# Performance work log

Hardware: AMD Instinct MI355X
Metric: run time of the kernel (lower is better)

## Reference

```python
import jax, jax.numpy as jnp
import numpy as np

B, S, D = 8, 2048, 512  # batch, seq_len, dim_val == dim_attn

def setup_inputs() -> dict:
    key = jax.random.key(0)
    kx, kq, kk, kv = jax.random.split(key, 4)
    scale = 1.0 / np.sqrt(D)
    return {
        "x": jax.random.normal(kx, (B, S, D), dtype=jnp.float32),
        "Wq": jax.random.normal(kq, (D, D), dtype=jnp.float32) * scale,  # dim_input -> dim_attn
        "Wk": jax.random.normal(kk, (D, D), dtype=jnp.float32) * scale,
        "Wv": jax.random.normal(kv, (D, D), dtype=jnp.float32) * scale,  # dim_input -> dim_val
    }

def reference(x, Wq, Wk, Wv):
    # bias-free linear projections (nn.Linear stores W as [out,in]; here W is [in,out])
    Q = jnp.einsum("bsd,de->bse", x, Wq)
    K = jnp.einsum("bsd,de->bse", x, Wk)
    V = jnp.einsum("bsd,de->bse", x, Wv)
    # manual scaled dot-product attention: softmax(QK^T / sqrt(d_attn)) V
    scores = jnp.einsum("bqe,bke->bqk", Q, K) / jnp.sqrt(jnp.asarray(Q.shape[-1], Q.dtype))
    a = jax.nn.softmax(scores, axis=-1)
    return jnp.einsum("bqk,bkd->bqd", a, V)
```

## Files before the change

### kernel.cpp

```cpp
#include <hip/hip_runtime.h>


typedef __attribute__((ext_vector_type(8))) short bf16x8;
typedef __attribute__((ext_vector_type(4))) short short4v;
typedef __attribute__((ext_vector_type(4))) float f32x4;
typedef __attribute__((ext_vector_type(16))) float f32x16;

__device__ __forceinline__ short f2bf(float f) {
  union { float f; unsigned u; } v; v.f = f;
  unsigned r = v.u + 0x7fffu + ((v.u >> 16) & 1u);
  return (short)(r >> 16);
}

__device__ __forceinline__ float exp2_raw(float x) {
  float r;
  asm("v_exp_f32 %0, %1" : "=v"(r) : "v"(x));
  return r;
}

__global__ __launch_bounds__(256) void prep_kernel(const float* __restrict__ x,
                                                   const float* __restrict__ Wq,
                                                   const float* __restrict__ Wk,
                                                   const float* __restrict__ Wv,
                                                   short* __restrict__ WT,
                                                   short* __restrict__ xb) {
  if (blockIdx.x < 384) {
    int g = blockIdx.x * 256 + threadIdx.x;
    int w = g >> 15;
    int rem = g & 32767;
    int n = rem & 511;
    int k0 = (rem >> 9) << 3;
    const float* W = (w == 0) ? Wq : ((w == 1) ? Wk : Wv);
    bf16x8 o;
#pragma unroll
    for (int j = 0; j < 8; ++j) o[j] = f2bf(W[(k0 + j) * 512 + n]);
    *(bf16x8*)(WT + w * 262144 + n * 512 + k0) = o;
  } else {
    size_t g = (size_t)(blockIdx.x - 384) * 256 + threadIdx.x;
    size_t off = g * 8;
    f32x4 lo = *(const f32x4*)(x + off);
    f32x4 hi = *(const f32x4*)(x + off + 4);
    bf16x8 o;
    o[0] = f2bf(lo[0]); o[1] = f2bf(lo[1]); o[2] = f2bf(lo[2]); o[3] = f2bf(lo[3]);
    o[4] = f2bf(hi[0]); o[5] = f2bf(hi[1]); o[6] = f2bf(hi[2]); o[7] = f2bf(hi[3]);
    *(bf16x8*)(xb + off) = o;
  }
}

__global__ __launch_bounds__(256, 2) void proj_kernel(const short* __restrict__ xb,
                                                      const short* __restrict__ WT,
                                                      short* __restrict__ QP,
                                                      short* __restrict__ KP,
                                                      short* __restrict__ VP) {
  __shared__ __align__(16) short Tb[8704];

  const int tid = threadIdx.x, wv = tid >> 6, ln = tid & 63;
  const int lane_m = ln & 15, lane_q = ln >> 4;
  const int m0 = blockIdx.x * 128, n0 = blockIdx.y * 64;
  const int wm = wv & 1, wn = wv >> 1;

  const short* ap[4];
#pragma unroll
  for (int mi = 0; mi < 4; ++mi)
    ap[mi] = xb + (size_t)(m0 + (wm * 4 + mi) * 16 + lane_m) * 512 + lane_q * 8;
  const short* bp[3][2];
#pragma unroll
  for (int z = 0; z < 3; ++z)
#pragma unroll
    for (int nj = 0; nj < 2; ++nj)
      bp[z][nj] = WT + z * 262144 + (size_t)(n0 + (wn * 2 + nj) * 16 + lane_m) * 512 + lane_q * 8;

  f32x4 zero4 = {0.f, 0.f, 0.f, 0.f};
  f32x4 acc[3][4][2];
#pragma unroll
  for (int z = 0; z < 3; ++z)
#pragma unroll
    for (int i = 0; i < 4; ++i)
#pragma unroll
      for (int j = 0; j < 2; ++j) acc[z][i][j] = zero4;

#pragma unroll
  for (int kk = 0; kk < 16; ++kk) {
    const int ko = kk * 32;
    bf16x8 a[4];
#pragma unroll
    for (int mi = 0; mi < 4; ++mi) a[mi] = *(const bf16x8*)(ap[mi] + ko);
    bf16x8 b[3][2];
#pragma unroll
    for (int z = 0; z < 3; ++z)
#pragma unroll
      for (int nj = 0; nj < 2; ++nj) b[z][nj] = *(const bf16x8*)(bp[z][nj] + ko);
#pragma unroll
    for (int z = 0; z < 3; ++z)
#pragma unroll
      for (int mi = 0; mi < 4; ++mi) {
        acc[z][mi][0] = __builtin_amdgcn_mfma_f32_16x16x32_bf16(a[mi], b[z][0], acc[z][mi][0], 0, 0, 0);
        acc[z][mi][1] = __builtin_amdgcn_mfma_f32_16x16x32_bf16(a[mi], b[z][1], acc[z][mi][1], 0, 0, 0);
      }
  }

  const int bb = m0 >> 11;

#pragma unroll
  for (int z = 0; z < 2; ++z) {
    __syncthreads();
#pragma unroll
    for (int mi = 0; mi < 4; ++mi)
#pragma unroll
      for (int nj = 0; nj < 2; ++nj)
#pragma unroll
        for (int rr = 0; rr < 4; ++rr)
          Tb[(wm * 64 + mi * 16 + lane_q * 4 + rr) * 68 + wn * 32 + nj * 16 + lane_m] =
              f2bf(acc[z][mi][nj][rr]);
    __syncthreads();
    short* Odst = (z == 0) ? QP : KP;
    const int g0 = (m0 & 2047) >> 5, kst0 = n0 >> 4;
#pragma unroll
    for (int p = 0; p < 4; ++p) {
      const int c2 = p * 256 + tid;
      const int frag = c2 >> 6, ln2 = c2 & 63;
      const int gl = frag >> 2, kl = frag & 3;
      const short* src = Tb + (gl * 32 + (ln2 & 31)) * 68 + kl * 16 + ((ln2 >> 5) << 3);
      size_t dst = (size_t)bb * 1048576 + (size_t)((g0 + gl) * 32 + kst0 + kl) * 512 + ln2 * 8;
      *(bf16x8*)(Odst + dst) = *(const bf16x8*)src;
    }
  }
  {
    __syncthreads();
#pragma unroll
    for (int mi = 0; mi < 4; ++mi)
#pragma unroll
      for (int nj = 0; nj < 2; ++nj)
#pragma unroll
        for (int rr = 0; rr < 4; ++rr)
          Tb[(wn * 32 + nj * 16 + lane_m) * 132 + wm * 64 + mi * 16 + lane_q * 4 + rr] =
              f2bf(acc[2][mi][nj][rr]);
    __syncthreads();
    const int ng0 = n0 >> 5, kv0 = (m0 & 2047) >> 4;
#pragma unroll
    for (int p = 0; p < 4; ++p) {
      const int c2 = p * 256 + tid;
      const int frag = c2 >> 6, ln2 = c2 & 63;
      const int ngl = frag >> 3, kvl = frag & 7;
      const short* src = Tb + (ngl * 32 + (ln2 & 31)) * 132 + kvl * 16 + ((ln2 >> 5) << 3);
      size_t dst = (size_t)bb * 1048576 + (size_t)((ng0 + ngl) * 128 + kv0 + kvl) * 512 + ln2 * 8;
      *(bf16x8*)(VP + dst) = *(const bf16x8*)src;
    }
  }
}


#define ISSUE8(R, a0_, a1_, B)                                               \
  asm volatile("global_load_dwordx4 %0, %8, %10\n\t"                         \
               "global_load_dwordx4 %1, %8, %10 offset:1024\n\t"             \
               "global_load_dwordx4 %2, %8, %10 offset:2048\n\t"             \
               "global_load_dwordx4 %3, %8, %10 offset:3072\n\t"             \
               "global_load_dwordx4 %4, %9, %10\n\t"                         \
               "global_load_dwordx4 %5, %9, %10 offset:1024\n\t"             \
               "global_load_dwordx4 %6, %9, %10 offset:2048\n\t"             \
               "global_load_dwordx4 %7, %9, %10 offset:3072\n\t"             \
               : "=&v"(R[0]), "=&v"(R[1]), "=&v"(R[2]), "=&v"(R[3]),         \
                 "=&v"(R[4]), "=&v"(R[5]), "=&v"(R[6]), "=&v"(R[7])          \
               : "v"(a0_), "v"(a1_), "s"(B))

#define WAIT8(R, N)                                                          \
  asm volatile("s_waitcnt vmcnt(" #N ")"                                     \
               : "+v"(R[0]), "+v"(R[1]), "+v"(R[2]), "+v"(R[3]),             \
                 "+v"(R[4]), "+v"(R[5]), "+v"(R[6]), "+v"(R[7]))

#define MFMA32(A, B, C) __builtin_amdgcn_mfma_f32_32x32x16_bf16(A, B, C, 0, 0, 0)

#define ISSUE_KQ(X, kt_, qq)                                                 \
  { const unsigned a0 = kb0 + (unsigned)(((kt_) & 7) * 262144) + (qq) * 8192u; \
    ISSUE8(X, a0, a0 + 4096u, Kp); }

#define ISSUE_VQ(X, kt_, bb_)                                                \
  { const unsigned a0 = vb0 + (unsigned)((kt_) * 16384) + (bb_) * 4096u;     \
    ISSUE8(X, a0, a0 + 131072u, VTp); }

#define S_PHASE(X, ph)                                                       \
  WAIT8(X, 8);                                                               \
  __builtin_amdgcn_s_setprio(1);                                             \
  _Pragma("unroll")                                                          \
  for (int c = 0; c < 8; ++c) {                                              \
    const int kst = (ph) * 8 + c;                                            \
    bf16x8 q0 = *(bf16x8*)(qf + kst * 512 + ln * 8);                         \
    bf16x8 q1 = *(bf16x8*)(qf + (32 + kst) * 512 + ln * 8);                  \
    s0 = MFMA32(X[c], q0, s0);                                               \
    s1 = MFMA32(X[c], q1, s1);                                               \
  }                                                                          \
  __builtin_amdgcn_s_setprio(0);

#define PF_RD(qh_, kv_)                                                      \
  (*(bf16x8*)(pfb + (qh_) * 8192 + q32 * 256 + ((((kv_) * 16) + hq8) ^ sw3)))

#define PV_PHASE(X, bb_)                                                     \
  WAIT8(X, 8);                                                               \
  __builtin_amdgcn_s_setprio(1);                                             \
  _Pragma("unroll")                                                          \
  for (int c = 0; c < 4; ++c) {                                              \
    const int kv = (bb_) * 4 + c;                                            \
    bf16x8 p0 = PF_RD(0, kv);                                                \
    bf16x8 p1 = PF_RD(1, kv);                                                \
    O00 = MFMA32(X[c], p0, O00);                                             \
    O01 = MFMA32(X[c], p1, O01);                                             \
    O10 = MFMA32(X[4 + c], p0, O10);                                         \
    O11 = MFMA32(X[4 + c], p1, O11);                                         \
  }                                                                          \
  __builtin_amdgcn_s_setprio(0);

__global__ __launch_bounds__(512, 2) void flash_kernel(const short* __restrict__ Q,
                                                       const short* __restrict__ K,
                                                       const short* __restrict__ VT,
                                                       float* __restrict__ out) {
  __shared__ __align__(16) short qf[32768];
  __shared__ __align__(16) short pf[32768];
  __shared__ float l_red[8][64];
  __shared__ float lsum[64];

  const int tid = threadIdx.x, w = tid >> 6, ln = tid & 63;
  const int q32 = ln & 31, hq = ln >> 5;
  const int hq8 = hq * 8, hq4 = hq * 4;
  const int sw3 = (q32 & 7) << 3;
  const int b = blockIdx.x & 7, qt = blockIdx.x >> 3;
  const int m0 = qt * 64;
  const short* Qp = Q + (size_t)b * 1048576;
  const short* Kp = K + (size_t)b * 1048576;
  const short* VTp = VT + (size_t)b * 1048576;
  const float sc2 = 0.044194173824159216f * 1.4426950408889634f;

#pragma unroll
  for (int r = 0; r < 8; ++r) {
    const int reg = w * 8 + r;
    *(bf16x8*)(qf + reg * 512 + ln * 8) =
        *(const bf16x8*)(Qp + (size_t)(qt * 64 + reg) * 512 + ln * 8);
  }

  f32x16 zz = {};
  f32x16 O00 = zz, O01 = zz, O10 = zz, O11 = zz;
  float lp0 = 0.f, lp1 = 0.f;

  const unsigned kb0 = (unsigned)(w * 32768 + ln * 16);
  const unsigned vb0 = (unsigned)(w * 262144 + ln * 16);

  __syncthreads();

  bf16x8 kX[8], kY[8], vA[8], vB[8];
  ISSUE_KQ(kX, 0, 0);
  ISSUE_KQ(kY, 0, 1);

#pragma unroll 1
  for (int kt = 0; kt < 8; ++kt) {
    f32x16 s0 = zz, s1 = zz;
    short* pfb = pf + (kt & 1) * 16384;

    S_PHASE(kX, 0); ISSUE_KQ(kX, kt, 2);
    S_PHASE(kY, 1); ISSUE_KQ(kY, kt, 3);
    S_PHASE(kX, 2); ISSUE_VQ(vA, kt, 0);
    S_PHASE(kY, 3); ISSUE_VQ(vB, kt, 1);

#pragma unroll
    for (int g2 = 0; g2 < 4; ++g2) {
      float a0 = exp2_raw(s0[g2 * 4 + 0] * sc2 - 12.0f);
      float a1 = exp2_raw(s0[g2 * 4 + 1] * sc2 - 12.0f);
      float a2 = exp2_raw(s0[g2 * 4 + 2] * sc2 - 12.0f);
      float a3 = exp2_raw(s0[g2 * 4 + 3] * sc2 - 12.0f);
      lp0 += (a0 + a1) + (a2 + a3);
      short4v v0c = {f2bf(a0), f2bf(a1), f2bf(a2), f2bf(a3)};
      *(short4v*)(pfb + q32 * 256 + (((w * 32 + g2 * 8) + hq4) ^ sw3)) = v0c;
      float c0 = exp2_raw(s1[g2 * 4 + 0] * sc2 - 12.0f);
      float c1 = exp2_raw(s1[g2 * 4 + 1] * sc2 - 12.0f);
      float c2 = exp2_raw(s1[g2 * 4 + 2] * sc2 - 12.0f);
      float c3 = exp2_raw(s1[g2 * 4 + 3] * sc2 - 12.0f);
      lp1 += (c0 + c1) + (c2 + c3);
      short4v v1c = {f2bf(c0), f2bf(c1), f2bf(c2), f2bf(c3)};
      *(short4v*)(pfb + 8192 + q32 * 256 + (((w * 32 + g2 * 8) + hq4) ^ sw3)) = v1c;
    }
    asm volatile("s_waitcnt lgkmcnt(0)" ::: "memory");
    __builtin_amdgcn_s_barrier();
    asm volatile("" ::: "memory");

    PV_PHASE(vA, 0); ISSUE_VQ(vA, kt, 2);
    PV_PHASE(vB, 1); ISSUE_VQ(vB, kt, 3);
    PV_PHASE(vA, 2); ISSUE_KQ(kX, kt + 1, 0);
    PV_PHASE(vB, 3); ISSUE_KQ(kY, kt + 1, 1);
  }
  WAIT8(kX, 8);
  WAIT8(kY, 0);

  lp0 += __shfl_xor(lp0, 32);
  lp1 += __shfl_xor(lp1, 32);
  if (ln < 32) {
    l_red[w][q32] = lp0;
    l_red[w][32 + q32] = lp1;
  }
  __syncthreads();
  if (tid < 64) {
    float s = 0.f;
#pragma unroll
    for (int ww = 0; ww < 8; ++ww) s += l_red[ww][tid];
    lsum[tid] = s;
  }
  __syncthreads();

  const float li0 = 1.f / lsum[q32];
  const float li1 = 1.f / lsum[32 + q32];
#pragma unroll
  for (int g2 = 0; g2 < 4; ++g2) {
    const int dq = g2 * 8 + hq4;
    const size_t r0 = ((size_t)b * 2048 + m0 + q32) * 512 + w * 64;
    const size_t r1 = ((size_t)b * 2048 + m0 + 32 + q32) * 512 + w * 64;
    f32x4 o;
    o[0] = O00[g2 * 4 + 0] * li0; o[1] = O00[g2 * 4 + 1] * li0;
    o[2] = O00[g2 * 4 + 2] * li0; o[3] = O00[g2 * 4 + 3] * li0;
    *(f32x4*)(out + r0 + dq) = o;
    o[0] = O10[g2 * 4 + 0] * li0; o[1] = O10[g2 * 4 + 1] * li0;
    o[2] = O10[g2 * 4 + 2] * li0; o[3] = O10[g2 * 4 + 3] * li0;
    *(f32x4*)(out + r0 + 32 + dq) = o;
    o[0] = O01[g2 * 4 + 0] * li1; o[1] = O01[g2 * 4 + 1] * li1;
    o[2] = O01[g2 * 4 + 2] * li1; o[3] = O01[g2 * 4 + 3] * li1;
    *(f32x4*)(out + r1 + dq) = o;
    o[0] = O11[g2 * 4 + 0] * li1; o[1] = O11[g2 * 4 + 1] * li1;
    o[2] = O11[g2 * 4 + 2] * li1; o[3] = O11[g2 * 4 + 3] * li1;
    *(f32x4*)(out + r1 + 32 + dq) = o;
  }
}

extern "C" void kernel_launch(void* const* d_in, const int* in_sizes, int n_in,
                              void* d_out, int out_size, void* d_ws, size_t ws_size,
                              hipStream_t stream) {
  const float* x  = (const float*)d_in[0];
  const float* Wq = (const float*)d_in[1];
  const float* Wk = (const float*)d_in[2];
  const float* Wv = (const float*)d_in[3];
  float* out = (float*)d_out;
  char* ws = (char*)d_ws;
  short* WT = (short*)ws;
  short* QP = (short*)(ws + 1572864);
  short* KP = (short*)(ws + 1572864 + 16777216);
  short* VP = (short*)(ws + 1572864 + 2 * 16777216);
  short* xb = (short*)(ws + 1572864 + 3 * 16777216);

  prep_kernel<<<dim3(384 + 4096), dim3(256), 0, stream>>>(x, Wq, Wk, Wv, WT, xb);
  proj_kernel<<<dim3(128, 8), dim3(256), 0, stream>>>(xb, WT, QP, KP, VP);
  flash_kernel<<<dim3(256), dim3(512), 0, stream>>>(QP, KP, VP, out);
}
```

Baseline: 234.0 us.

## Pre-pack x and weights into MFMA fragment layout and use 32x32x16 MFMA in projection

The prep kernel now writes x and the transposed weights in a fragment-packed layout, so each wave in the projection kernel reads a contiguous 1 KB chunk per k-step with a single coalesced 16-byte load per lane. The projection kernel switches from 16x16x32 to 32x32x16 bf16 MFMA, with each wave owning a 32-row slab across all 64 output columns for Q, K and V. This cuts the strided global loads and the MFMA instruction count. Each A fragment is now loaded once per wave instead of being shared across the wn split, and the accumulator epilogue is remapped to the 32x32 register layout.

```diff
diff --git a/kernel.cpp b/kernel.cpp
--- a/kernel.cpp
+++ b/kernel.cpp
@@ -22,128 +22,119 @@
                                                    const float* __restrict__ Wq,
                                                    const float* __restrict__ Wk,
                                                    const float* __restrict__ Wv,
-                                                   short* __restrict__ WT,
-                                                   short* __restrict__ xb) {
+                                                   short* __restrict__ WTP,
+                                                   short* __restrict__ xbp) {
   if (blockIdx.x < 384) {
     int g = blockIdx.x * 256 + threadIdx.x;
-    int w = g >> 15;
+    int z = g >> 15;
     int rem = g & 32767;
-    int n = rem & 511;
-    int k0 = (rem >> 9) << 3;
-    const float* W = (w == 0) ? Wq : ((w == 1) ? Wk : Wv);
+    int c = rem >> 6, ln2 = rem & 63;
+    int gc = c >> 5, kst = c & 31;
+    const float* W = (z == 0) ? Wq : ((z == 1) ? Wk : Wv);
+    const int col = gc * 32 + (ln2 & 31);
+    const int k0 = kst * 16 + ((ln2 >> 5) << 3);
     bf16x8 o;
 #pragma unroll
-    for (int j = 0; j < 8; ++j) o[j] = f2bf(W[(k0 + j) * 512 + n]);
-    *(bf16x8*)(WT + w * 262144 + n * 512 + k0) = o;
+    for (int j = 0; j < 8; ++j) o[j] = f2bf(W[(k0 + j) * 512 + col]);
+    *(bf16x8*)(WTP + z * 262144 + c * 512 + ln2 * 8) = o;
   } else {
-    size_t g = (size_t)(blockIdx.x - 384) * 256 + threadIdx.x;
-    size_t off = g * 8;
-    f32x4 lo = *(const f32x4*)(x + off);
-    f32x4 hi = *(const f32x4*)(x + off + 4);
+    int t = (blockIdx.x - 384) * 256 + threadIdx.x;
+    const int r = t >> 6;
+    const int d0 = (t & 63) * 8;
+    f32x4 lo = *(const f32x4*)(x + (size_t)r * 512 + d0);
+    f32x4 hi = *(const f32x4*)(x + (size_t)r * 512 + d0 + 4);
     bf16x8 o;
     o[0] = f2bf(lo[0]); o[1] = f2bf(lo[1]); o[2] = f2bf(lo[2]); o[3] = f2bf(lo[3]);
     o[4] = f2bf(hi[0]); o[5] = f2bf(hi[1]); o[6] = f2bf(hi[2]); o[7] = f2bf(hi[3]);
-    *(bf16x8*)(xb + off) = o;
-  }
-}
-
-__global__ __launch_bounds__(256, 2) void proj_kernel(const short* __restrict__ xb,
-                                                      const short* __restrict__ WT,
+    const int gg = r >> 5, l31 = r & 31;
+    const int kst = d0 >> 4, hq2 = (d0 >> 3) & 1;
+    *(bf16x8*)(xbp + (size_t)(gg * 32 + kst) * 512 + (hq2 * 32 + l31) * 8) = o;
+  }
+}
+
+__global__ __launch_bounds__(256, 2) void proj_kernel(const short* __restrict__ xbp,
+                                                      const short* __restrict__ WTP,
                                                       short* __restrict__ QP,
                                                       short* __restrict__ KP,
                                                       short* __restrict__ VP) {
   __shared__ __align__(16) short Tb[8704];
 
   const int tid = threadIdx.x, wv = tid >> 6, ln = tid & 63;
-  const int lane_m = ln & 15, lane_q = ln >> 4;
+  const int q32 = ln & 31, hq = ln >> 5;
   const int m0 = blockIdx.x * 128, n0 = blockIdx.y * 64;
-  const int wm = wv & 1, wn = wv >> 1;
-
-  const short* ap[4];
-#pragma unroll
-  for (int mi = 0; mi < 4; ++mi)
-    ap[mi] = xb + (size_t)(m0 + (wm * 4 + mi) * 16 + lane_m) * 512 + lane_q * 8;
-  const short* bp[3][2];
+
+  const short* apt = xbp + (size_t)(((m0 >> 5) + wv) * 32) * 512 + ln * 8;
+  const short* bpt[3][2];
 #pragma unroll
   for (int z = 0; z < 3; ++z)
 #pragma unroll
     for (int nj = 0; nj < 2; ++nj)
-      bp[z][nj] = WT + z * 262144 + (size_t)(n0 + (wn * 2 + nj) * 16 + lane_m) * 512 + lane_q * 8;
-
-  f32x4 zero4 = {0.f, 0.f, 0.f, 0.f};
-  f32x4 acc[3][4][2];
-#pragma unroll
-  for (int z = 0; z < 3; ++z)
-#pragma unroll
-    for (int i = 0; i < 4; ++i)
-#pragma unroll
-      for (int j = 0; j < 2; ++j) acc[z][i][j] = zero4;
-
-#pragma unroll
-  for (int kk = 0; kk < 16; ++kk) {
-    const int ko = kk * 32;
-    bf16x8 a[4];
-#pragma unroll
-    for (int mi = 0; mi < 4; ++mi) a[mi] = *(const bf16x8*)(ap[mi] + ko);
-    bf16x8 b[3][2];
-#pragma unroll
-    for (int z = 0; z < 3; ++z)
-#pragma unroll
-      for (int nj = 0; nj < 2; ++nj) b[z][nj] = *(const bf16x8*)(bp[z][nj] + ko);
-#pragma unroll
-    for (int z = 0; z < 3; ++z)
-#pragma unroll
-      for (int mi = 0; mi < 4; ++mi) {
-        acc[z][mi][0] = __builtin_amdgcn_mfma_f32_16x16x32_bf16(a[mi], b[z][0], acc[z][mi][0], 0, 0, 0);
-        acc[z][mi][1] = __builtin_amdgcn_mfma_f32_16x16x32_bf16(a[mi], b[z][1], acc[z][mi][1], 0, 0, 0);
-      }
-  }
-
-  const int bb = m0 >> 11;
+      bpt[z][nj] = WTP + z * 262144 + (size_t)(((n0 >> 5) + nj) * 32) * 512 + ln * 8;
+
+  f32x16 zz = {};
+  f32x16 acc[3][2];
+#pragma unroll
+  for (int z = 0; z < 3; ++z) { acc[z][0] = zz; acc[z][1] = zz; }
+
+#pragma unroll
+  for (int kst = 0; kst < 32; ++kst) {
+    bf16x8 a = *(const bf16x8*)(apt + kst * 512);
+    bf16x8 b00 = *(const bf16x8*)(bpt[0][0] + kst * 512);
+    bf16x8 b01 = *(const bf16x8*)(bpt[0][1] + kst * 512);
+    bf16x8 b10 = *(const bf16x8*)(bpt[1][0] + kst * 512);
+    bf16x8 b11 = *(const bf16x8*)(bpt[1][1] + kst * 512);
+    bf16x8 b20 = *(const bf16x8*)(bpt[2][0] + kst * 512);
+    bf16x8 b21 = *(const bf16x8*)(bpt[2][1] + kst * 512);
+    acc[0][0] = __builtin_amdgcn_mfma_f32_32x32x16_bf16(a, b00, acc[0][0], 0, 0, 0);
+    acc[0][1] = __builtin_amdgcn_mfma_f32_32x32x16_bf16(a, b01, acc[0][1], 0, 0, 0);
+    acc[1][0] = __builtin_amdgcn_mfma_f32_32x32x16_bf16(a, b10, acc[1][0], 0, 0, 0);
+    acc[1][1] = __builtin_amdgcn_mfma_f32_32x32x16_bf16(a, b11, acc[1][1], 0, 0, 0);
+    acc[2][0] = __builtin_amdgcn_mfma_f32_32x32x16_bf16(a, b20, acc[2][0], 0, 0, 0);
+    acc[2][1] = __builtin_amdgcn_mfma_f32_32x32x16_bf16(a, b21, acc[2][1], 0, 0, 0);
+  }
 
 #pragma unroll
   for (int z = 0; z < 2; ++z) {
     __syncthreads();
 #pragma unroll
-    for (int mi = 0; mi < 4; ++mi)
-#pragma unroll
-      for (int nj = 0; nj < 2; ++nj)
-#pragma unroll
-        for (int rr = 0; rr < 4; ++rr)
-          Tb[(wm * 64 + mi * 16 + lane_q * 4 + rr) * 68 + wn * 32 + nj * 16 + lane_m] =
-              f2bf(acc[z][mi][nj][rr]);
+    for (int nj = 0; nj < 2; ++nj)
+#pragma unroll
+      for (int reg = 0; reg < 16; ++reg) {
+        const int mloc = wv * 32 + (reg & 3) + 8 * (reg >> 2) + 4 * hq;
+        Tb[mloc * 68 + nj * 32 + q32] = f2bf(acc[z][nj][reg]);
+      }
     __syncthreads();
     short* Odst = (z == 0) ? QP : KP;
-    const int g0 = (m0 & 2047) >> 5, kst0 = n0 >> 4;
+    const int kst0 = n0 >> 4;
 #pragma unroll
     for (int p = 0; p < 4; ++p) {
       const int c2 = p * 256 + tid;
       const int frag = c2 >> 6, ln2 = c2 & 63;
       const int gl = frag >> 2, kl = frag & 3;
       const short* src = Tb + (gl * 32 + (ln2 & 31)) * 68 + kl * 16 + ((ln2 >> 5) << 3);
-      size_t dst = (size_t)bb * 1048576 + (size_t)((g0 + gl) * 32 + kst0 + kl) * 512 + ln2 * 8;
+      size_t dst = ((size_t)((m0 >> 5) + gl) * 32 + kst0 + kl) * 512 + ln2 * 8;
       *(bf16x8*)(Odst + dst) = *(const bf16x8*)src;
     }
   }
   {
     __syncthreads();
 #pragma unroll
-    for (int mi = 0; mi < 4; ++mi)
-#pragma unroll
-      for (int nj = 0; nj < 2; ++nj)
-#pragma unroll
-        for (int rr = 0; rr < 4; ++rr)
-          Tb[(wn * 32 + nj * 16 + lane_m) * 132 + wm * 64 + mi * 16 + lane_q * 4 + rr] =
-              f2bf(acc[2][mi][nj][rr]);
+    for (int nj = 0; nj < 2; ++nj)
+#pragma unroll
+      for (int reg = 0; reg < 16; ++reg) {
+        const int mloc = wv * 32 + (reg & 3) + 8 * (reg >> 2) + 4 * hq;
+        Tb[(nj * 32 + q32) * 132 + mloc] = f2bf(acc[2][nj][reg]);
+      }
     __syncthreads();
     const int ng0 = n0 >> 5, kv0 = (m0 & 2047) >> 4;
+    const size_t vbase = (size_t)(m0 >> 11) * 1048576;
 #pragma unroll
     for (int p = 0; p < 4; ++p) {
       const int c2 = p * 256 + tid;
       const int frag = c2 >> 6, ln2 = c2 & 63;
       const int ngl = frag >> 3, kvl = frag & 7;
       const short* src = Tb + (ngl * 32 + (ln2 & 31)) * 132 + kvl * 16 + ((ln2 >> 5) << 3);
-      size_t dst = (size_t)bb * 1048576 + (size_t)((ng0 + ngl) * 128 + kv0 + kvl) * 512 + ln2 * 8;
+      size_t dst = vbase + (size_t)((ng0 + ngl) * 128 + kv0 + kvl) * 512 + ln2 * 8;
       *(bf16x8*)(VP + dst) = *(const bf16x8*)src;
     }
   }
@@ -335,13 +326,13 @@
   const float* Wv = (const float*)d_in[3];
   float* out = (float*)d_out;
   char* ws = (char*)d_ws;
-  short* WT = (short*)ws;
+  short* WTP = (short*)ws;
   short* QP = (short*)(ws + 1572864);
   short* KP = (short*)(ws + 1572864 + 16777216);
   short* VP = (short*)(ws + 1572864 + 2 * 16777216);
-  short* xb = (short*)(ws + 1572864 + 3 * 16777216);
-
-  prep_kernel<<<dim3(384 + 4096), dim3(256), 0, stream>>>(x, Wq, Wk, Wv, WT, xb);
-  proj_kernel<<<dim3(128, 8), dim3(256), 0, stream>>>(xb, WT, QP, KP, VP);
+  short* xbp = (short*)(ws + 1572864 + 3 * 16777216);
+
+  prep_kernel<<<dim3(384 + 4096), dim3(256), 0, stream>>>(x, Wq, Wk, Wv, WTP, xbp);
+  proj_kernel<<<dim3(128, 8), dim3(256), 0, stream>>>(xbp, WTP, QP, KP, VP);
   flash_kernel<<<dim3(256), dim3(512), 0, stream>>>(QP, KP, VP, out);
 }
```

Result: slower. 253.3 us (+8.2%).
